# Optimization experiments

Measured on AMD Instinct MI355X. Metric: run time of the kernel, lower is better.

## Reference

```python
import jax, jax.numpy as jnp
import numpy as np

V, B, S, DI, DH, DO = 32000, 32, 512, 256, 512, 128


def setup_inputs() -> dict:
    key = jax.random.key(0)
    ks = jax.random.split(key, 10)
    w = lambda k, shape: (jax.random.normal(k, shape, jnp.float32) * 0.02)
    z = lambda n: jnp.zeros((n,), jnp.float32)
    return {
        "tokens": jax.random.randint(ks[0], (B, S), 0, V, dtype=jnp.int32),
        "emb": w(ks[1], (V, DI)),
        "l0_Wz": w(ks[2], (DI + DH, DH)), "l0_bz": z(DH),
        "l0_Wr": w(ks[3], (DI + DH, DH)), "l0_br": z(DH),
        "l0_Wn": w(ks[4], (DI + DH, DH)), "l0_bn": z(DH),
        "l1_Wz": w(ks[5], (DH + DH, DH)), "l1_bz": z(DH),
        "l1_Wr": w(ks[6], (DH + DH, DH)), "l1_br": z(DH),
        "l1_Wn": w(ks[7], (DH + DH, DH)), "l1_bn": z(DH),
        "fc_W": w(ks[8], (DH, DO)), "fc_b": z(DO),
    }


def gru_layer(x_seq, Wz, bz, Wr, br, Wn, bn):
    # x_seq: [B, S, Din]; hidden dim inferred from Wz
    dh = Wz.shape[1]
    h0 = jnp.zeros((x_seq.shape[0], dh), x_seq.dtype)

    def step(H, x_t):
        comb = jnp.concatenate([x_t, H], axis=-1)          # [B, Din+DH]
        Z = jax.nn.sigmoid(comb @ Wz + bz)
        Rg = jax.nn.sigmoid(comb @ Wr + br)
        comb2 = jnp.concatenate([x_t, Rg * H], axis=-1)
        H_tilde = jnp.tanh(comb2 @ Wn + bn)
        Hn = (1.0 - Z) * H + Z * H_tilde
        return Hn, Hn

    _, ys = jax.lax.scan(step, h0, jnp.swapaxes(x_seq, 0, 1))  # [S, B, DH]
    return jnp.swapaxes(ys, 0, 1)                              # [B, S, DH]


def reference(tokens, emb,
              l0_Wz, l0_bz, l0_Wr, l0_br, l0_Wn, l0_bn,
              l1_Wz, l1_bz, l1_Wr, l1_br, l1_Wn, l1_bn,
              fc_W, fc_b):
    x = emb[tokens]                                            # [B, S, DI]
    x = gru_layer(x, l0_Wz, l0_bz, l0_Wr, l0_br, l0_Wn, l0_bn)
    x = gru_layer(x, l1_Wz, l1_bz, l1_Wr, l1_br, l1_Wn, l1_bn)
    logits = x @ fc_W + fc_b                                   # [B, S, DO]
    return jax.nn.log_softmax(logits, axis=-1)
```

## Files before the change

### kernel.cpp

```cpp
#include <hip/hip_runtime.h>
#include <hip/hip_bf16.h>
#include <cstdint>
#include <cstddef>


typedef short v8ss __attribute__((ext_vector_type(8)));
typedef float v4f  __attribute__((ext_vector_type(4)));
typedef unsigned short u16x8 __attribute__((ext_vector_type(8)));
typedef unsigned long long u64;

#define MFMA16(a, b, c) __builtin_amdgcn_mfma_f32_16x16x32_bf16((a), (b), (c), 0, 0, 0)

__device__ __forceinline__ unsigned short f2bf(float f) {
  union { float f; unsigned u; } v; v.f = f;
  unsigned r = v.u + 0x7fffu + ((v.u >> 16) & 1u);
  return (unsigned short)(r >> 16);
}
__device__ __forceinline__ unsigned short f2bfp(float f) {
  unsigned short h = f2bf(f);
  return (h == 0x8080u) ? (unsigned short)0x8081u : h;
}
__device__ __forceinline__ float bf2f(unsigned short h) {
  union { unsigned u; float f; } v; v.u = ((unsigned)h) << 16; return v.f;
}

#define S64   0x8080808080808080ull
#define INF64 0x7F807F807F807F80ull
#define POLL_LIM 65536

__device__ __forceinline__ u64 aload(const u64* p) {
  return __hip_atomic_load(p, __ATOMIC_RELAXED, __HIP_MEMORY_SCOPE_AGENT);
}
__device__ __forceinline__ void astore(u64* p, u64 v) {
  __hip_atomic_store(p, v, __ATOMIC_RELAXED, __HIP_MEMORY_SCOPE_AGENT);
}
__device__ __forceinline__ void spin2(const u64* p, u64* o, int* dead) {
  u64 a = aload(p), b = aload(p + 1);
  int it = 0;
  while ((a == S64) | (b == S64)) {
    if (*(volatile int*)dead) break;
    if (++it > POLL_LIM) { *(volatile int*)dead = 1; break; }
    if (it > 4) __builtin_amdgcn_s_sleep(1);
    a = aload(p); b = aload(p + 1);
  }
  o[0] = a; o[1] = b;
}
__device__ __forceinline__ void spin4(const u64* p, u64* o, int* dead) {
  u64 a = aload(p), b = aload(p + 1), c = aload(p + 2), d = aload(p + 3);
  int it = 0;
  while ((a == S64) | (b == S64) | (c == S64) | (d == S64)) {
    if (*(volatile int*)dead) break;
    if (++it > POLL_LIM) { *(volatile int*)dead = 1; break; }
    if (it > 4) __builtin_amdgcn_s_sleep(1);
    a = aload(p); b = aload(p + 1); c = aload(p + 2); d = aload(p + 3);
  }
  o[0] = a; o[1] = b; o[2] = c; o[3] = d;
}
__device__ __forceinline__ void spin22(const u64* p, const u64* q, u64* o, int* dead) {
  u64 a = aload(p), b = aload(p + 1), c = aload(q), d = aload(q + 1);
  int it = 0;
  while ((a == S64) | (b == S64) | (c == S64) | (d == S64)) {
    if (*(volatile int*)dead) break;
    if (++it > POLL_LIM) { *(volatile int*)dead = 1; break; }
    if (it > 4) __builtin_amdgcn_s_sleep(1);
    a = aload(p); b = aload(p + 1); c = aload(q); d = aload(q + 1);
  }
  o[0] = a; o[1] = b; o[2] = c; o[3] = d;
}
__device__ __forceinline__ void chunk2lds(unsigned short* base, int col, u64 v) {
  base[col]            = (unsigned short)v;
  base[520 + col]      = (unsigned short)(v >> 16);
  base[2 * 520 + col]  = (unsigned short)(v >> 32);
  base[3 * 520 + col]  = (unsigned short)(v >> 48);
}

#define BB   32
#define SS   512
#define DI   256
#define DH   512
#define DO   128
#define MROWS (BB * SS)
#define SLAB 16384

#define O_HX0   0
#define O_HX1   16809984
#define O_RHX0  33619968
#define O_RHX1  50397184
#define O_Y1    67174400
#define O_WT0X  (O_Y1 + (size_t)MROWS*DH*2)
#define O_WT0H  (O_WT0X + 1536*256*2)
#define O_WT1X  (O_WT0H + 16*96*512*2)
#define O_WT1H  (O_WT1X + 1536*512*2)
#define O_WTFC  (O_WT1H + 16*96*512*2)
#define O_XEMB  (O_WTFC + 128*512*2)

__global__ void prep_kernel(const float* __restrict__ l0Wz, const float* __restrict__ l0Wr,
                            const float* __restrict__ l0Wn,
                            const float* __restrict__ l1Wz, const float* __restrict__ l1Wr,
                            const float* __restrict__ l1Wn,
                            const float* __restrict__ fcW,
                            unsigned short* __restrict__ Wt0x, unsigned short* __restrict__ Wt0h,
                            unsigned short* __restrict__ Wt1x, unsigned short* __restrict__ Wt1h,
                            unsigned short* __restrict__ WtFC) {
  const int n0 = 1536 * 256;
  const int n1 = 16 * 96 * 512;
  const int n2 = 1536 * 512;
  const int n3 = 16 * 96 * 512;
  const int n4 = 128 * 512;
  const int total = n0 + n1 + n2 + n3 + n4;
  for (int i = blockIdx.x * 256 + threadIdx.x; i < total; i += gridDim.x * 256) {
    int j = i;
    if (j < n0) {
      int gcol = j / 256, k = j % 256, g = gcol >> 9, c = gcol & 511;
      const float* W = g == 0 ? l0Wz : (g == 1 ? l0Wr : l0Wn);
      Wt0x[j] = f2bf(W[k * 512 + c]); continue;
    }
    j -= n0;
    if (j < n1) {
      int r = j / (96 * 512), rem = j % (96 * 512), row = rem / 512, k = rem % 512;
      int g = row >> 5, c = r * 32 + (row & 31);
      const float* W = g == 0 ? l0Wz : (g == 1 ? l0Wr : l0Wn);
      Wt0h[j] = f2bf(W[(256 + k) * 512 + c]); continue;
    }
    j -= n1;
    if (j < n2) {
      int gcol = j / 512, k = j % 512, g = gcol >> 9, c = gcol & 511;
      const float* W = g == 0 ? l1Wz : (g == 1 ? l1Wr : l1Wn);
      Wt1x[j] = f2bf(W[k * 512 + c]); continue;
    }
    j -= n2;
    if (j < n3) {
      int r = j / (96 * 512), rem = j % (96 * 512), row = rem / 512, k = rem % 512;
      int g = row >> 5, c = r * 32 + (row & 31);
      const float* W = g == 0 ? l1Wz : (g == 1 ? l1Wr : l1Wn);
      Wt1h[j] = f2bf(W[(512 + k) * 512 + c]); continue;
    }
    j -= n3;
    { int c = j / 512, k = j % 512; WtFC[j] = f2bf(fcW[k * 128 + c]); }
  }
}

__global__ void embed_kernel(const int* __restrict__ tokens, const float* __restrict__ emb,
                             unsigned short* __restrict__ Xemb) {
  int r = blockIdx.x;
  int c = threadIdx.x;
  int t = r >> 5, b = r & 31;
  int tok = tokens[b * SS + t];
  Xemb[(size_t)r * DI + c] = f2bf(emb[(size_t)tok * DI + c]);
}

template <int LAYER>
__device__ __forceinline__ void gru_body(
    const int g, const int role, const int tid,
    const unsigned short* __restrict__ WtH,
    const unsigned short* __restrict__ Wx,
    const unsigned short* __restrict__ Xe,
    unsigned short* hx0,
    unsigned short* hx, unsigned short* rhx,
    unsigned short* Y1,
    const float* __restrict__ bz, const float* __restrict__ br,
    const float* __restrict__ bn,
    unsigned short* Wt, unsigned short* At, unsigned short* Rt, unsigned short* Xt,
    float* zbuf, float* hbuf, int* dead) {
  constexpr int K = LAYER ? 512 : 256;

  for (int ch = tid; ch < 96 * 64; ch += 256) {
    int row = ch >> 6, off = (ch & 63) * 8;
    *(u16x8*)&Wt[row * 520 + off] = *(const u16x8*)&WtH[((size_t)role * 96 + row) * 512 + off];
  }
  for (int i = tid * 8; i < 16 * 520; i += 256 * 8) {
    *(u16x8*)&At[i] = (u16x8)0;
    *(u16x8*)&Rt[i] = (u16x8)0;
    *(u16x8*)&Xt[i] = (u16x8)0;
  }
  if (tid < 128) { zbuf[tid] = 0.f; hbuf[tid] = 0.f; }
  __syncthreads();

  const int w = tid >> 6, l = tid & 63, cl = l & 15, kg = l >> 4;
  const int gate = w >> 1;
  const int lc16 = (w & 1) * 16;
  const int colA = role * 32 + lc16 + cl;
  const float biasA = (gate ? br : bz)[colA];
  const int lc16b = (w & 1) * 16;
  const int colB = role * 32 + lc16b + cl;
  const float biasB = (w < 2) ? bn[colB] : 0.f;

  const size_t gofs = (size_t)g * 2048;
  const int tt = tid & 127;
  const unsigned short* WxA = Wx + (size_t)(gate * 512 + colA) * K;
  const unsigned short* WxB = Wx + (size_t)(1024 + colB) * K;

  for (int t = 0; t < SS; ++t) {
    if (LAYER == 0) {
      u16x8 xreg;
      if (tid < 128) {
        int j = tid >> 5, off = (tid & 31) * 8;
        xreg = *(const u16x8*)&Xe[((size_t)(t * 32) + 4 * g + j) * 256 + off];
      }
      u64 o[2];
      spin2((const u64*)(hx + (size_t)t * SLAB + gofs) + tid * 2, o, dead);
      chunk2lds(At, tid * 2, o[0]);
      chunk2lds(At, tid * 2 + 1, o[1]);
      if (tid < 128) {
        int j = tid >> 5, off = (tid & 31) * 8;
        *(u16x8*)&Xt[j * 520 + off] = xreg;
      }
    } else {
      u64 o[4];
      spin22((const u64*)(hx0 + (size_t)(t + 1) * SLAB + gofs) + tid * 2,
             (const u64*)(hx + (size_t)t * SLAB + gofs) + tid * 2, o, dead);
      chunk2lds(Xt, tid * 2, o[0]);
      chunk2lds(Xt, tid * 2 + 1, o[1]);
      chunk2lds(At, tid * 2, o[2]);
      chunk2lds(At, tid * 2 + 1, o[3]);
    }
    __syncthreads();
    if (*(volatile int*)dead) break;

    {
      v4f acc = {};
#pragma unroll
      for (int kc = 0; kc < K / 32; ++kc) {
        int ko = kc * 32 + kg * 8;
        v8ss a = *(const v8ss*)&Xt[cl * 520 + ko];
        v8ss b = *(const v8ss*)&WxA[ko];
        acc = MFMA16(a, b, acc);
      }
#pragma unroll
      for (int kc = 0; kc < 16; ++kc) {
        int ko = kc * 32 + kg * 8;
        v8ss a = *(const v8ss*)&At[cl * 520 + ko];
        v8ss b = *(const v8ss*)&Wt[(gate * 32 + lc16 + cl) * 520 + ko];
        acc = MFMA16(a, b, acc);
      }
      if (l < 16) {
        if (gate == 0) {
#pragma unroll
          for (int j = 0; j < 4; ++j) {
            float pre = acc[j] + biasA;
            zbuf[j * 32 + lc16 + cl] = 1.f / (1.f + __expf(-pre));
          }
        } else {
          u64 pk = 0;
#pragma unroll
          for (int j = 0; j < 4; ++j) {
            float pre = acc[j] + biasA;
            float gv = 1.f / (1.f + __expf(-pre));
            pk |= (u64)f2bfp(gv * hbuf[j * 32 + lc16 + cl]) << (16 * j);
          }
          astore((u64*)(rhx + (size_t)t * SLAB + gofs) + colA, pk);
        }
      }
    }
    v4f accB = {};
    if (w >= 2) {
      u64 o[4];
      spin4((const u64*)(rhx + (size_t)t * SLAB + gofs) + tt * 4, o, dead);
      chunk2lds(Rt, tt * 4, o[0]);
      chunk2lds(Rt, tt * 4 + 1, o[1]);
      chunk2lds(Rt, tt * 4 + 2, o[2]);
      chunk2lds(Rt, tt * 4 + 3, o[3]);
    } else {
#pragma unroll
      for (int kc = 0; kc < K / 32; ++kc) {
        int ko = kc * 32 + kg * 8;
        v8ss a = *(const v8ss*)&Xt[cl * 520 + ko];
        v8ss b = *(const v8ss*)&WxB[ko];
        accB = MFMA16(a, b, accB);
      }
    }
    __syncthreads();
    if (*(volatile int*)dead) break;

    if (w < 2) {
#pragma unroll
      for (int kc = 0; kc < 16; ++kc) {
        int ko = kc * 32 + kg * 8;
        v8ss a = *(const v8ss*)&Rt[cl * 520 + ko];
        v8ss b = *(const v8ss*)&Wt[(64 + lc16b + cl) * 520 + ko];
        accB = MFMA16(a, b, accB);
      }
      if (l < 16) {
        int lc = lc16b + cl;
        u64 pk = 0;
        unsigned short hv[4];
#pragma unroll
        for (int j = 0; j < 4; ++j) {
          float pre = accB[j] + biasB;
          float ht = 1.f - 2.f / (__expf(2.f * pre) + 1.f);
          float z = zbuf[j * 32 + lc];
          float hn = (1.f - z) * hbuf[j * 32 + lc] + z * ht;
          hbuf[j * 32 + lc] = hn;
          hv[j] = f2bfp(hn);
          pk |= (u64)hv[j] << (16 * j);
        }
        astore((u64*)(hx + (size_t)(t + 1) * SLAB + gofs) + colB, pk);
        if (LAYER == 1) {
#pragma unroll
          for (int j = 0; j < 4; ++j)
            Y1[((size_t)(t * 32) + 4 * g + j) * 512 + colB] = hv[j];
        }
      }
    }
    __syncthreads();
  }

  if (*(volatile int*)dead) {
    for (int s = tid; s < SS * 32; s += 256) {
      int t2 = s >> 5, c = role * 32 + (s & 31);
      astore((u64*)(hx + (size_t)(t2 + 1) * SLAB + gofs) + c, INF64);
      astore((u64*)(rhx + (size_t)t2 * SLAB + gofs) + c, INF64);
    }
  }
}

__global__ __launch_bounds__(256, 1) void gru_fused(
    const unsigned short* __restrict__ Wt0h, const unsigned short* __restrict__ Wt1h,
    const unsigned short* __restrict__ Wt0x, const unsigned short* __restrict__ Wt1x,
    const unsigned short* __restrict__ Xemb,
    unsigned short* hx0, unsigned short* rhx0,
    unsigned short* hx1, unsigned short* rhx1,
    unsigned short* Y1,
    const float* bz0, const float* br0, const float* bn0,
    const float* bz1, const float* br1, const float* bn1) {
  __shared__ unsigned short Wt[96 * 520];
  __shared__ unsigned short At[16 * 520];
  __shared__ unsigned short Rt[16 * 520];
  __shared__ unsigned short Xt[16 * 520];
  __shared__ float zbuf[128], hbuf[128];
  __shared__ int dead;
  const int tid = threadIdx.x;
  if (tid == 0) dead = 0;
  const int layer = blockIdx.x >> 7, id = blockIdx.x & 127;
  const int g = id >> 4, role = id & 15;
  if (layer == 0)
    gru_body<0>(g, role, tid, Wt0h, Wt0x, Xemb, nullptr, hx0, rhx0, nullptr,
                bz0, br0, bn0, Wt, At, Rt, Xt, zbuf, hbuf, &dead);
  else
    gru_body<1>(g, role, tid, Wt1h, Wt1x, nullptr, hx0, hx1, rhx1, Y1,
                bz1, br1, bn1, Wt, At, Rt, Xt, zbuf, hbuf, &dead);
}

__global__ __launch_bounds__(256) void fc_lsm_kernel(const unsigned short* __restrict__ Y1,
                                                     const unsigned short* __restrict__ WtFC,
                                                     const float* __restrict__ fcb,
                                                     float* __restrict__ out) {
  __shared__ float lout[32 * 128];
  int w = threadIdx.x >> 6, l = threadIdx.x & 63;
  int cl = l & 15, kg = l >> 4;
  int m0 = blockIdx.x * 32, n0 = w * 32;
  v4f acc[2][2] = {};
#pragma unroll
  for (int kc = 0; kc < 16; ++kc) {
    int ko = kc * 32 + kg * 8;
    v8ss a0 = *(const v8ss*)&Y1[(size_t)(m0 + cl) * 512 + ko];
    v8ss a1 = *(const v8ss*)&Y1[(size_t)(m0 + 16 + cl) * 512 + ko];
    v8ss b0 = *(const v8ss*)&WtFC[(size_t)(n0 + cl) * 512 + ko];
    v8ss b1 = *(const v8ss*)&WtFC[(size_t)(n0 + 16 + cl) * 512 + ko];
    acc[0][0] = MFMA16(a0, b0, acc[0][0]);
    acc[0][1] = MFMA16(a0, b1, acc[0][1]);
    acc[1][0] = MFMA16(a1, b0, acc[1][0]);
    acc[1][1] = MFMA16(a1, b1, acc[1][1]);
  }
#pragma unroll
  for (int mi = 0; mi < 2; ++mi)
#pragma unroll
    for (int ni = 0; ni < 2; ++ni) {
      int col = n0 + ni * 16 + cl;
      float bias = fcb[col];
#pragma unroll
      for (int r = 0; r < 4; ++r)
        lout[(mi * 16 + kg * 4 + r) * 128 + col] = acc[mi][ni][r] + bias;
    }
  __syncthreads();

  for (int rr = 0; rr < 8; ++rr) {
    int lr = w * 8 + rr;
    float a = lout[lr * 128 + l], b2 = lout[lr * 128 + 64 + l];
    float m = fmaxf(a, b2);
#pragma unroll
    for (int off = 32; off; off >>= 1) m = fmaxf(m, __shfl_xor(m, off));
    float s = __expf(a - m) + __expf(b2 - m);
#pragma unroll
    for (int off = 32; off; off >>= 1) s += __shfl_xor(s, off);
    float lse = m + logf(s);
    int mrow = m0 + lr, t = mrow >> 5, bb = mrow & 31;
    float* o = &out[((size_t)bb * SS + t) * 128];
    o[l] = a - lse;
    o[l + 64] = b2 - lse;
  }
}

extern "C" void kernel_launch(void* const* d_in, const int* in_sizes, int n_in,
                              void* d_out, int out_size, void* d_ws, size_t ws_size,
                              hipStream_t stream) {
  (void)in_sizes; (void)n_in; (void)out_size; (void)ws_size;
  const int*   tokens = (const int*)d_in[0];
  const float* emb    = (const float*)d_in[1];
  const float* l0Wz = (const float*)d_in[2];  const float* l0bz = (const float*)d_in[3];
  const float* l0Wr = (const float*)d_in[4];  const float* l0br = (const float*)d_in[5];
  const float* l0Wn = (const float*)d_in[6];  const float* l0bn = (const float*)d_in[7];
  const float* l1Wz = (const float*)d_in[8];  const float* l1bz = (const float*)d_in[9];
  const float* l1Wr = (const float*)d_in[10]; const float* l1br = (const float*)d_in[11];
  const float* l1Wn = (const float*)d_in[12]; const float* l1bn = (const float*)d_in[13];
  const float* fcW  = (const float*)d_in[14]; const float* fcb  = (const float*)d_in[15];

  char* ws = (char*)d_ws;
  unsigned short* hx0  = (unsigned short*)(ws + O_HX0);
  unsigned short* hx1  = (unsigned short*)(ws + O_HX1);
  unsigned short* rhx0 = (unsigned short*)(ws + O_RHX0);
  unsigned short* rhx1 = (unsigned short*)(ws + O_RHX1);
  unsigned short* Y1   = (unsigned short*)(ws + O_Y1);
  unsigned short* Wt0x = (unsigned short*)(ws + O_WT0X);
  unsigned short* Wt0h = (unsigned short*)(ws + O_WT0H);
  unsigned short* Wt1x = (unsigned short*)(ws + O_WT1X);
  unsigned short* Wt1h = (unsigned short*)(ws + O_WT1H);
  unsigned short* WtFC = (unsigned short*)(ws + O_WTFC);
  unsigned short* Xemb = (unsigned short*)(ws + O_XEMB);

  hipMemsetAsync(hx0, 0x00, 32768, stream);
  hipMemsetAsync((char*)hx0 + 32768, 0x80, (size_t)SS * 32768, stream);
  hipMemsetAsync(hx1, 0x00, 32768, stream);
  hipMemsetAsync((char*)hx1 + 32768, 0x80, (size_t)SS * 32768, stream);
  hipMemsetAsync(rhx0, 0x80, (size_t)SS * 32768, stream);
  hipMemsetAsync(rhx1, 0x80, (size_t)SS * 32768, stream);

  prep_kernel<<<4096, 256, 0, stream>>>(l0Wz, l0Wr, l0Wn, l1Wz, l1Wr, l1Wn, fcW,
                                        Wt0x, Wt0h, Wt1x, Wt1h, WtFC);
  embed_kernel<<<MROWS, 256, 0, stream>>>(tokens, emb, Xemb);

  gru_fused<<<256, 256, 0, stream>>>(Wt0h, Wt1h, Wt0x, Wt1x, Xemb,
                                     hx0, rhx0, hx1, rhx1, Y1,
                                     l0bz, l0br, l0bn, l1bz, l1br, l1bn);

  fc_lsm_kernel<<<512, 256, 0, stream>>>(Y1, WtFC, fcb, (float*)d_out);
}
```

Before: 3.120 ms.

## Remove block barriers from GRU step by making each wave load state redundantly

```diff
diff --git a/kernel.cpp b/kernel.cpp
--- a/kernel.cpp
+++ b/kernel.cpp
@@ -34,38 +34,39 @@
 __device__ __forceinline__ void astore(u64* p, u64 v) {
   __hip_atomic_store(p, v, __ATOMIC_RELAXED, __HIP_MEMORY_SCOPE_AGENT);
 }
-__device__ __forceinline__ void spin2(const u64* p, u64* o, int* dead) {
-  u64 a = aload(p), b = aload(p + 1);
-  int it = 0;
-  while ((a == S64) | (b == S64)) {
-    if (*(volatile int*)dead) break;
-    if (++it > POLL_LIM) { *(volatile int*)dead = 1; break; }
+__device__ __forceinline__ void spin8x(const u64* p, u64* o, int* dead) {
+#pragma unroll
+  for (int i = 0; i < 8; ++i) o[i] = aload(p + i);
+  for (int it = 0;; ++it) {
+    int any = 0;
+#pragma unroll
+    for (int i = 0; i < 8; ++i) any |= (o[i] == S64);
+    if (!any) return;
+    if (*(volatile int*)dead) return;
+    if (it > POLL_LIM) { *(volatile int*)dead = 1; return; }
     if (it > 4) __builtin_amdgcn_s_sleep(1);
-    a = aload(p); b = aload(p + 1);
-  }
-  o[0] = a; o[1] = b;
-}
-__device__ __forceinline__ void spin4(const u64* p, u64* o, int* dead) {
-  u64 a = aload(p), b = aload(p + 1), c = aload(p + 2), d = aload(p + 3);
-  int it = 0;
-  while ((a == S64) | (b == S64) | (c == S64) | (d == S64)) {
-    if (*(volatile int*)dead) break;
-    if (++it > POLL_LIM) { *(volatile int*)dead = 1; break; }
+#pragma unroll
+    for (int i = 0; i < 8; ++i) if (o[i] == S64) o[i] = aload(p + i);
+  }
+}
+__device__ __forceinline__ void spin88(const u64* p, const u64* q, u64* o, int* dead) {
+#pragma unroll
+  for (int i = 0; i < 8; ++i) o[i] = aload(p + i);
+#pragma unroll
+  for (int i = 0; i < 8; ++i) o[8 + i] = aload(q + i);
+  for (int it = 0;; ++it) {
+    int any = 0;
+#pragma unroll
+    for (int i = 0; i < 16; ++i) any |= (o[i] == S64);
+    if (!any) return;
+    if (*(volatile int*)dead) return;
+    if (it > POLL_LIM) { *(volatile int*)dead = 1; return; }
     if (it > 4) __builtin_amdgcn_s_sleep(1);
-    a = aload(p); b = aload(p + 1); c = aload(p + 2); d = aload(p + 3);
-  }
-  o[0] = a; o[1] = b; o[2] = c; o[3] = d;
-}
-__device__ __forceinline__ void spin22(const u64* p, const u64* q, u64* o, int* dead) {
-  u64 a = aload(p), b = aload(p + 1), c = aload(q), d = aload(q + 1);
-  int it = 0;
-  while ((a == S64) | (b == S64) | (c == S64) | (d == S64)) {
-    if (*(volatile int*)dead) break;
-    if (++it > POLL_LIM) { *(volatile int*)dead = 1; break; }
-    if (it > 4) __builtin_amdgcn_s_sleep(1);
-    a = aload(p); b = aload(p + 1); c = aload(q); d = aload(q + 1);
-  }
-  o[0] = a; o[1] = b; o[2] = c; o[3] = d;
+#pragma unroll
+    for (int i = 0; i < 8; ++i) if (o[i] == S64) o[i] = aload(p + i);
+#pragma unroll
+    for (int i = 0; i < 8; ++i) if (o[8 + i] == S64) o[8 + i] = aload(q + i);
+  }
 }
 __device__ __forceinline__ void chunk2lds(unsigned short* base, int col, u64 v) {
   base[col]            = (unsigned short)v;
@@ -161,7 +162,7 @@
     const float* __restrict__ bz, const float* __restrict__ br,
     const float* __restrict__ bn,
     unsigned short* Wt, unsigned short* At, unsigned short* Rt, unsigned short* Xt,
-    float* zbuf, float* hbuf, int* dead) {
+    int* dead) {
   constexpr int K = LAYER ? 512 : 256;
 
   for (int ch = tid; ch < 96 * 64; ch += 256) {
@@ -173,136 +174,121 @@
     *(u16x8*)&Rt[i] = (u16x8)0;
     *(u16x8*)&Xt[i] = (u16x8)0;
   }
-  if (tid < 128) { zbuf[tid] = 0.f; hbuf[tid] = 0.f; }
   __syncthreads();
 
   const int w = tid >> 6, l = tid & 63, cl = l & 15, kg = l >> 4;
-  const int gate = w >> 1;
-  const int lc16 = (w & 1) * 16;
-  const int colA = role * 32 + lc16 + cl;
-  const float biasA = (gate ? br : bz)[colA];
-  const int lc16b = (w & 1) * 16;
-  const int colB = role * 32 + lc16b + cl;
-  const float biasB = (w < 2) ? bn[colB] : 0.f;
-
+  const int isR = (w >= 2), wsub = isR ? (w - 2) : w;
+  const int col = role * 32 + 16 * wsub + cl;
+  const float biasZ = bz[col], biasR = br[col], biasN = bn[col];
+  const unsigned short* WxZ = Wx + (size_t)col * K;
+  const unsigned short* WxR = Wx + (size_t)(512 + col) * K;
+  const unsigned short* WxN = Wx + (size_t)(1024 + col) * K;
   const size_t gofs = (size_t)g * 2048;
-  const int tt = tid & 127;
-  const unsigned short* WxA = Wx + (size_t)(gate * 512 + colA) * K;
-  const unsigned short* WxB = Wx + (size_t)(1024 + colB) * K;
+  v4f hreg = {};
 
   for (int t = 0; t < SS; ++t) {
+    if (*(volatile int*)dead) break;
     if (LAYER == 0) {
-      u16x8 xreg;
-      if (tid < 128) {
-        int j = tid >> 5, off = (tid & 31) * 8;
-        xreg = *(const u16x8*)&Xe[((size_t)(t * 32) + 4 * g + j) * 256 + off];
-      }
-      u64 o[2];
-      spin2((const u64*)(hx + (size_t)t * SLAB + gofs) + tid * 2, o, dead);
-      chunk2lds(At, tid * 2, o[0]);
-      chunk2lds(At, tid * 2 + 1, o[1]);
-      if (tid < 128) {
-        int j = tid >> 5, off = (tid & 31) * 8;
-        *(u16x8*)&Xt[j * 520 + off] = xreg;
-      }
+      int s0 = l * 2, r0 = s0 >> 5, of0 = (s0 & 31) * 8;
+      int s1 = s0 + 1, r1 = s1 >> 5, of1 = (s1 & 31) * 8;
+      u16x8 x0 = *(const u16x8*)&Xe[((size_t)(t * 32) + 4 * g + r0) * 256 + of0];
+      u16x8 x1 = *(const u16x8*)&Xe[((size_t)(t * 32) + 4 * g + r1) * 256 + of1];
+      u64 o[8];
+      spin8x((const u64*)(hx + (size_t)t * SLAB + gofs) + l * 8, o, dead);
+#pragma unroll
+      for (int i = 0; i < 8; ++i) chunk2lds(At, l * 8 + i, o[i]);
+      *(u16x8*)&Xt[r0 * 520 + of0] = x0;
+      *(u16x8*)&Xt[r1 * 520 + of1] = x1;
     } else {
-      u64 o[4];
-      spin22((const u64*)(hx0 + (size_t)(t + 1) * SLAB + gofs) + tid * 2,
-             (const u64*)(hx + (size_t)t * SLAB + gofs) + tid * 2, o, dead);
-      chunk2lds(Xt, tid * 2, o[0]);
-      chunk2lds(Xt, tid * 2 + 1, o[1]);
-      chunk2lds(At, tid * 2, o[2]);
-      chunk2lds(At, tid * 2 + 1, o[3]);
-    }
-    __syncthreads();
-    if (*(volatile int*)dead) break;
-
-    {
+      u64 o[16];
+      spin88((const u64*)(hx0 + (size_t)(t + 1) * SLAB + gofs) + l * 8,
+             (const u64*)(hx + (size_t)t * SLAB + gofs) + l * 8, o, dead);
+#pragma unroll
+      for (int i = 0; i < 8; ++i) chunk2lds(Xt, l * 8 + i, o[i]);
+#pragma unroll
+      for (int i = 0; i < 8; ++i) chunk2lds(At, l * 8 + i, o[8 + i]);
+    }
+    asm volatile("s_waitcnt lgkmcnt(0)" ::: "memory");
+    __builtin_amdgcn_sched_barrier(0);
+
+    if (isR) {
       v4f acc = {};
 #pragma unroll
       for (int kc = 0; kc < K / 32; ++kc) {
         int ko = kc * 32 + kg * 8;
-        v8ss a = *(const v8ss*)&Xt[cl * 520 + ko];
-        v8ss b = *(const v8ss*)&WxA[ko];
-        acc = MFMA16(a, b, acc);
+        acc = MFMA16(*(const v8ss*)&Xt[cl * 520 + ko], *(const v8ss*)&WxR[ko], acc);
       }
 #pragma unroll
       for (int kc = 0; kc < 16; ++kc) {
         int ko = kc * 32 + kg * 8;
-        v8ss a = *(const v8ss*)&At[cl * 520 + ko];
-        v8ss b = *(const v8ss*)&Wt[(gate * 32 + lc16 + cl) * 520 + ko];
-        acc = MFMA16(a, b, acc);
+        acc = MFMA16(*(const v8ss*)&At[cl * 520 + ko],
+                     *(const v8ss*)&Wt[(32 + 16 * wsub + cl) * 520 + ko], acc);
       }
       if (l < 16) {
-        if (gate == 0) {
-#pragma unroll
-          for (int j = 0; j < 4; ++j) {
-            float pre = acc[j] + biasA;
-            zbuf[j * 32 + lc16 + cl] = 1.f / (1.f + __expf(-pre));
-          }
-        } else {
-          u64 pk = 0;
-#pragma unroll
-          for (int j = 0; j < 4; ++j) {
-            float pre = acc[j] + biasA;
-            float gv = 1.f / (1.f + __expf(-pre));
-            pk |= (u64)f2bfp(gv * hbuf[j * 32 + lc16 + cl]) << (16 * j);
-          }
-          astore((u64*)(rhx + (size_t)t * SLAB + gofs) + colA, pk);
+        u64 pk = 0;
+#pragma unroll
+        for (int j = 0; j < 4; ++j) {
+          float gv = 1.f / (1.f + __expf(-(acc[j] + biasR)));
+          float h = bf2f(At[j * 520 + col]);
+          pk |= (u64)f2bfp(gv * h) << (16 * j);
         }
-      }
-    }
-    v4f accB = {};
-    if (w >= 2) {
-      u64 o[4];
-      spin4((const u64*)(rhx + (size_t)t * SLAB + gofs) + tt * 4, o, dead);
-      chunk2lds(Rt, tt * 4, o[0]);
-      chunk2lds(Rt, tt * 4 + 1, o[1]);
-      chunk2lds(Rt, tt * 4 + 2, o[2]);
-      chunk2lds(Rt, tt * 4 + 3, o[3]);
+        astore((u64*)(rhx + (size_t)t * SLAB + gofs) + col, pk);
+      }
     } else {
+      v4f accZ = {};
 #pragma unroll
       for (int kc = 0; kc < K / 32; ++kc) {
         int ko = kc * 32 + kg * 8;
-        v8ss a = *(const v8ss*)&Xt[cl * 520 + ko];
-        v8ss b = *(const v8ss*)&WxB[ko];
-        accB = MFMA16(a, b, accB);
-      }
-    }
-    __syncthreads();
-    if (*(volatile int*)dead) break;
-
-    if (w < 2) {
+        accZ = MFMA16(*(const v8ss*)&Xt[cl * 520 + ko], *(const v8ss*)&WxZ[ko], accZ);
+      }
 #pragma unroll
       for (int kc = 0; kc < 16; ++kc) {
         int ko = kc * 32 + kg * 8;
-        v8ss a = *(const v8ss*)&Rt[cl * 520 + ko];
-        v8ss b = *(const v8ss*)&Wt[(64 + lc16b + cl) * 520 + ko];
-        accB = MFMA16(a, b, accB);
+        accZ = MFMA16(*(const v8ss*)&At[cl * 520 + ko],
+                      *(const v8ss*)&Wt[(16 * w + cl) * 520 + ko], accZ);
+      }
+      v4f z;
+#pragma unroll
+      for (int j = 0; j < 4; ++j) z[j] = 1.f / (1.f + __expf(-(accZ[j] + biasZ)));
+
+      v4f accB = {};
+#pragma unroll
+      for (int kc = 0; kc < K / 32; ++kc) {
+        int ko = kc * 32 + kg * 8;
+        accB = MFMA16(*(const v8ss*)&Xt[cl * 520 + ko], *(const v8ss*)&WxN[ko], accB);
+      }
+      u64 o2[8];
+      spin8x((const u64*)(rhx + (size_t)t * SLAB + gofs) + l * 8, o2, dead);
+#pragma unroll
+      for (int i = 0; i < 8; ++i) chunk2lds(Rt, l * 8 + i, o2[i]);
+      asm volatile("s_waitcnt lgkmcnt(0)" ::: "memory");
+      __builtin_amdgcn_sched_barrier(0);
+#pragma unroll
+      for (int kc = 0; kc < 16; ++kc) {
+        int ko = kc * 32 + kg * 8;
+        accB = MFMA16(*(const v8ss*)&Rt[cl * 520 + ko],
+                      *(const v8ss*)&Wt[(64 + 16 * w + cl) * 520 + ko], accB);
       }
       if (l < 16) {
-        int lc = lc16b + cl;
         u64 pk = 0;
         unsigned short hv[4];
 #pragma unroll
         for (int j = 0; j < 4; ++j) {
-          float pre = accB[j] + biasB;
+          float pre = accB[j] + biasN;
           float ht = 1.f - 2.f / (__expf(2.f * pre) + 1.f);
-          float z = zbuf[j * 32 + lc];
-          float hn = (1.f - z) * hbuf[j * 32 + lc] + z * ht;
-          hbuf[j * 32 + lc] = hn;
+          float hn = (1.f - z[j]) * hreg[j] + z[j] * ht;
+          hreg[j] = hn;
           hv[j] = f2bfp(hn);
           pk |= (u64)hv[j] << (16 * j);
         }
-        astore((u64*)(hx + (size_t)(t + 1) * SLAB + gofs) + colB, pk);
+        astore((u64*)(hx + (size_t)(t + 1) * SLAB + gofs) + col, pk);
         if (LAYER == 1) {
 #pragma unroll
           for (int j = 0; j < 4; ++j)
-            Y1[((size_t)(t * 32) + 4 * g + j) * 512 + colB] = hv[j];
+            Y1[((size_t)(t * 32) + 4 * g + j) * 512 + col] = hv[j];
         }
       }
     }
-    __syncthreads();
   }
 
   if (*(volatile int*)dead) {
@@ -327,7 +313,6 @@
   __shared__ unsigned short At[16 * 520];
   __shared__ unsigned short Rt[16 * 520];
   __shared__ unsigned short Xt[16 * 520];
-  __shared__ float zbuf[128], hbuf[128];
   __shared__ int dead;
   const int tid = threadIdx.x;
   if (tid == 0) dead = 0;
@@ -335,10 +320,10 @@
   const int g = id >> 4, role = id & 15;
   if (layer == 0)
     gru_body<0>(g, role, tid, Wt0h, Wt0x, Xemb, nullptr, hx0, rhx0, nullptr,
-                bz0, br0, bn0, Wt, At, Rt, Xt, zbuf, hbuf, &dead);
+                bz0, br0, bn0, Wt, At, Rt, Xt, &dead);
   else
     gru_body<1>(g, role, tid, Wt1h, Wt1x, nullptr, hx0, hx1, rhx1, Y1,
-                bz1, br1, bn1, Wt, At, Rt, Xt, zbuf, hbuf, &dead);
+                bz1, br1, bn1, Wt, At, Rt, Xt, &dead);
 }
 
 __global__ __launch_bounds__(256) void fc_lsm_kernel(const unsigned short* __restrict__ Y1,
```

Measured after the change: 5.190 ms. 1.66x slower.

## Precompute next-step input projections off the recurrent critical path in fused GRU

Applied to the files above, without the earlier changes.

```diff
diff --git a/kernel.cpp b/kernel.cpp
--- a/kernel.cpp
+++ b/kernel.cpp
@@ -53,17 +53,6 @@
     if (++it > POLL_LIM) { *(volatile int*)dead = 1; break; }
     if (it > 4) __builtin_amdgcn_s_sleep(1);
     a = aload(p); b = aload(p + 1); c = aload(p + 2); d = aload(p + 3);
-  }
-  o[0] = a; o[1] = b; o[2] = c; o[3] = d;
-}
-__device__ __forceinline__ void spin22(const u64* p, const u64* q, u64* o, int* dead) {
-  u64 a = aload(p), b = aload(p + 1), c = aload(q), d = aload(q + 1);
-  int it = 0;
-  while ((a == S64) | (b == S64) | (c == S64) | (d == S64)) {
-    if (*(volatile int*)dead) break;
-    if (++it > POLL_LIM) { *(volatile int*)dead = 1; break; }
-    if (it > 4) __builtin_amdgcn_s_sleep(1);
-    a = aload(p); b = aload(p + 1); c = aload(q); d = aload(q + 1);
   }
   o[0] = a; o[1] = b; o[2] = c; o[3] = d;
 }
@@ -161,7 +150,7 @@
     const float* __restrict__ bz, const float* __restrict__ br,
     const float* __restrict__ bn,
     unsigned short* Wt, unsigned short* At, unsigned short* Rt, unsigned short* Xt,
-    float* zbuf, float* hbuf, int* dead) {
+    int* dead) {
   constexpr int K = LAYER ? 512 : 256;
 
   for (int ch = tid; ch < 96 * 64; ch += 256) {
@@ -173,133 +162,158 @@
     *(u16x8*)&Rt[i] = (u16x8)0;
     *(u16x8*)&Xt[i] = (u16x8)0;
   }
-  if (tid < 128) { zbuf[tid] = 0.f; hbuf[tid] = 0.f; }
   __syncthreads();
 
   const int w = tid >> 6, l = tid & 63, cl = l & 15, kg = l >> 4;
-  const int gate = w >> 1;
+  const int isR = (w >= 2);
   const int lc16 = (w & 1) * 16;
-  const int colA = role * 32 + lc16 + cl;
-  const float biasA = (gate ? br : bz)[colA];
-  const int lc16b = (w & 1) * 16;
-  const int colB = role * 32 + lc16b + cl;
-  const float biasB = (w < 2) ? bn[colB] : 0.f;
-
+  const int col = role * 32 + lc16 + cl;
+  const float bZ = bz[col], bR = br[col], bN = bn[col];
+  const unsigned short* WxZ = Wx + (size_t)col * K;
+  const unsigned short* WxR = Wx + (size_t)(512 + col) * K;
+  const unsigned short* WxN = Wx + (size_t)(1024 + col) * K;
   const size_t gofs = (size_t)g * 2048;
   const int tt = tid & 127;
-  const unsigned short* WxA = Wx + (size_t)(gate * 512 + colA) * K;
-  const unsigned short* WxB = Wx + (size_t)(1024 + colB) * K;
+  v4f hreg = {};
+  v4f xZ = {}, xR = {}, xN = {};
+
+  if (LAYER == 0) {
+    if (tid < 128) {
+      int j = tid >> 5, off = (tid & 31) * 8;
+      *(u16x8*)&Xt[j * 520 + off] = *(const u16x8*)&Xe[((size_t)(4 * g) + j) * 256 + off];
+    }
+  } else {
+    u64 o[2];
+    spin2((const u64*)(hx0 + (size_t)1 * SLAB + gofs) + tid * 2, o, dead);
+    chunk2lds(Xt, tid * 2, o[0]);
+    chunk2lds(Xt, tid * 2 + 1, o[1]);
+  }
+  __syncthreads();
+  if (isR) {
+#pragma unroll
+    for (int kc = 0; kc < K / 32; ++kc) {
+      int ko = kc * 32 + kg * 8;
+      xR = MFMA16(*(const v8ss*)&Xt[cl * 520 + ko], *(const v8ss*)&WxR[ko], xR);
+    }
+  } else {
+#pragma unroll
+    for (int kc = 0; kc < K / 32; ++kc) {
+      int ko = kc * 32 + kg * 8;
+      xZ = MFMA16(*(const v8ss*)&Xt[cl * 520 + ko], *(const v8ss*)&WxZ[ko], xZ);
+      xN = MFMA16(*(const v8ss*)&Xt[cl * 520 + ko], *(const v8ss*)&WxN[ko], xN);
+    }
+  }
 
   for (int t = 0; t < SS; ++t) {
-    if (LAYER == 0) {
-      u16x8 xreg;
-      if (tid < 128) {
-        int j = tid >> 5, off = (tid & 31) * 8;
-        xreg = *(const u16x8*)&Xe[((size_t)(t * 32) + 4 * g + j) * 256 + off];
-      }
+    {
       u64 o[2];
       spin2((const u64*)(hx + (size_t)t * SLAB + gofs) + tid * 2, o, dead);
       chunk2lds(At, tid * 2, o[0]);
       chunk2lds(At, tid * 2 + 1, o[1]);
-      if (tid < 128) {
-        int j = tid >> 5, off = (tid & 31) * 8;
-        *(u16x8*)&Xt[j * 520 + off] = xreg;
-      }
-    } else {
-      u64 o[4];
-      spin22((const u64*)(hx0 + (size_t)(t + 1) * SLAB + gofs) + tid * 2,
-             (const u64*)(hx + (size_t)t * SLAB + gofs) + tid * 2, o, dead);
-      chunk2lds(Xt, tid * 2, o[0]);
-      chunk2lds(Xt, tid * 2 + 1, o[1]);
-      chunk2lds(At, tid * 2, o[2]);
-      chunk2lds(At, tid * 2 + 1, o[3]);
     }
     __syncthreads();
     if (*(volatile int*)dead) break;
 
-    {
-      v4f acc = {};
-#pragma unroll
-      for (int kc = 0; kc < K / 32; ++kc) {
-        int ko = kc * 32 + kg * 8;
-        v8ss a = *(const v8ss*)&Xt[cl * 520 + ko];
-        v8ss b = *(const v8ss*)&WxA[ko];
-        acc = MFMA16(a, b, acc);
-      }
+    v4f zreg;
+    if (isR) {
+      v4f acc = xR;
 #pragma unroll
       for (int kc = 0; kc < 16; ++kc) {
         int ko = kc * 32 + kg * 8;
-        v8ss a = *(const v8ss*)&At[cl * 520 + ko];
-        v8ss b = *(const v8ss*)&Wt[(gate * 32 + lc16 + cl) * 520 + ko];
-        acc = MFMA16(a, b, acc);
+        acc = MFMA16(*(const v8ss*)&At[cl * 520 + ko],
+                     *(const v8ss*)&Wt[(32 + lc16 + cl) * 520 + ko], acc);
       }
       if (l < 16) {
-        if (gate == 0) {
-#pragma unroll
-          for (int j = 0; j < 4; ++j) {
-            float pre = acc[j] + biasA;
-            zbuf[j * 32 + lc16 + cl] = 1.f / (1.f + __expf(-pre));
-          }
-        } else {
-          u64 pk = 0;
-#pragma unroll
-          for (int j = 0; j < 4; ++j) {
-            float pre = acc[j] + biasA;
-            float gv = 1.f / (1.f + __expf(-pre));
-            pk |= (u64)f2bfp(gv * hbuf[j * 32 + lc16 + cl]) << (16 * j);
-          }
-          astore((u64*)(rhx + (size_t)t * SLAB + gofs) + colA, pk);
+        u64 pk = 0;
+#pragma unroll
+        for (int j = 0; j < 4; ++j) {
+          float gv = 1.f / (1.f + __expf(-(acc[j] + bR)));
+          pk |= (u64)f2bfp(gv * bf2f(At[j * 520 + col])) << (16 * j);
         }
-      }
-    }
-    v4f accB = {};
-    if (w >= 2) {
+        astore((u64*)(rhx + (size_t)t * SLAB + gofs) + col, pk);
+      }
+    } else {
+      v4f acc = xZ;
+#pragma unroll
+      for (int kc = 0; kc < 16; ++kc) {
+        int ko = kc * 32 + kg * 8;
+        acc = MFMA16(*(const v8ss*)&At[cl * 520 + ko],
+                     *(const v8ss*)&Wt[(lc16 + cl) * 520 + ko], acc);
+      }
+#pragma unroll
+      for (int j = 0; j < 4; ++j) zreg[j] = 1.f / (1.f + __expf(-(acc[j] + bZ)));
+    }
+
+    if (isR) {
       u64 o[4];
       spin4((const u64*)(rhx + (size_t)t * SLAB + gofs) + tt * 4, o, dead);
       chunk2lds(Rt, tt * 4, o[0]);
       chunk2lds(Rt, tt * 4 + 1, o[1]);
       chunk2lds(Rt, tt * 4 + 2, o[2]);
       chunk2lds(Rt, tt * 4 + 3, o[3]);
-    } else {
-#pragma unroll
-      for (int kc = 0; kc < K / 32; ++kc) {
-        int ko = kc * 32 + kg * 8;
-        v8ss a = *(const v8ss*)&Xt[cl * 520 + ko];
-        v8ss b = *(const v8ss*)&WxB[ko];
-        accB = MFMA16(a, b, accB);
+    } else if (t + 1 < SS) {
+      if (LAYER == 0) {
+        int j = tid >> 5, off = (tid & 31) * 8;
+        *(u16x8*)&Xt[j * 520 + off] =
+            *(const u16x8*)&Xe[((size_t)((t + 1) * 32) + 4 * g + j) * 256 + off];
+      } else {
+        u64 o[4];
+        spin4((const u64*)(hx0 + (size_t)(t + 2) * SLAB + gofs) + tt * 4, o, dead);
+        chunk2lds(Xt, tt * 4, o[0]);
+        chunk2lds(Xt, tt * 4 + 1, o[1]);
+        chunk2lds(Xt, tt * 4 + 2, o[2]);
+        chunk2lds(Xt, tt * 4 + 3, o[3]);
       }
     }
     __syncthreads();
     if (*(volatile int*)dead) break;
 
-    if (w < 2) {
+    if (!isR) {
+      v4f acc = xN;
 #pragma unroll
       for (int kc = 0; kc < 16; ++kc) {
         int ko = kc * 32 + kg * 8;
-        v8ss a = *(const v8ss*)&Rt[cl * 520 + ko];
-        v8ss b = *(const v8ss*)&Wt[(64 + lc16b + cl) * 520 + ko];
-        accB = MFMA16(a, b, accB);
+        acc = MFMA16(*(const v8ss*)&Rt[cl * 520 + ko],
+                     *(const v8ss*)&Wt[(64 + lc16 + cl) * 520 + ko], acc);
       }
       if (l < 16) {
-        int lc = lc16b + cl;
         u64 pk = 0;
         unsigned short hv[4];
 #pragma unroll
         for (int j = 0; j < 4; ++j) {
-          float pre = accB[j] + biasB;
+          float pre = acc[j] + bN;
           float ht = 1.f - 2.f / (__expf(2.f * pre) + 1.f);
-          float z = zbuf[j * 32 + lc];
-          float hn = (1.f - z) * hbuf[j * 32 + lc] + z * ht;
-          hbuf[j * 32 + lc] = hn;
+          float hn = (1.f - zreg[j]) * hreg[j] + zreg[j] * ht;
+          hreg[j] = hn;
           hv[j] = f2bfp(hn);
           pk |= (u64)hv[j] << (16 * j);
         }
-        astore((u64*)(hx + (size_t)(t + 1) * SLAB + gofs) + colB, pk);
+        astore((u64*)(hx + (size_t)(t + 1) * SLAB + gofs) + col, pk);
         if (LAYER == 1) {
 #pragma unroll
           for (int j = 0; j < 4; ++j)
-            Y1[((size_t)(t * 32) + 4 * g + j) * 512 + colB] = hv[j];
+            Y1[((size_t)(t * 32) + 4 * g + j) * 512 + col] = hv[j];
         }
+      }
+      if (t + 1 < SS) {
+        v4f nz = {}, nn = {};
+#pragma unroll
+        for (int kc = 0; kc < K / 32; ++kc) {
+          int ko = kc * 32 + kg * 8;
+          nz = MFMA16(*(const v8ss*)&Xt[cl * 520 + ko], *(const v8ss*)&WxZ[ko], nz);
+          nn = MFMA16(*(const v8ss*)&Xt[cl * 520 + ko], *(const v8ss*)&WxN[ko], nn);
+        }
+        xZ = nz; xN = nn;
+      }
+    } else {
+      if (t + 1 < SS) {
+        v4f nr = {};
+#pragma unroll
+        for (int kc = 0; kc < K / 32; ++kc) {
+          int ko = kc * 32 + kg * 8;
+          nr = MFMA16(*(const v8ss*)&Xt[cl * 520 + ko], *(const v8ss*)&WxR[ko], nr);
+        }
+        xR = nr;
       }
     }
     __syncthreads();
@@ -327,7 +341,6 @@
   __shared__ unsigned short At[16 * 520];
   __shared__ unsigned short Rt[16 * 520];
   __shared__ unsigned short Xt[16 * 520];
-  __shared__ float zbuf[128], hbuf[128];
   __shared__ int dead;
   const int tid = threadIdx.x;
   if (tid == 0) dead = 0;
@@ -335,10 +348,10 @@
   const int g = id >> 4, role = id & 15;
   if (layer == 0)
     gru_body<0>(g, role, tid, Wt0h, Wt0x, Xemb, nullptr, hx0, rhx0, nullptr,
-                bz0, br0, bn0, Wt, At, Rt, Xt, zbuf, hbuf, &dead);
+                bz0, br0, bn0, Wt, At, Rt, Xt, &dead);
   else
     gru_body<1>(g, role, tid, Wt1h, Wt1x, nullptr, hx0, hx1, rhx1, Y1,
-                bz1, br1, bn1, Wt, At, Rt, Xt, zbuf, hbuf, &dead);
+                bz1, br1, bn1, Wt, At, Rt, Xt, &dead);
 }
 
 __global__ __launch_bounds__(256) void fc_lsm_kernel(const unsigned short* __restrict__ Y1,
```

New measurement: 3.130 ms. About the same (+0.3%).
